# Performance work log

Measured on AMD Instinct MI355X. Metric: run time of the kernel, lower is better.

The kernel has to match this reference:

```python
import jax, jax.numpy as jnp
import numpy as np


def setup_inputs() -> dict:
    key = jax.random.key(0)
    k1, k2, k3, k4 = jax.random.split(key, 4)
    B, D, N, M = 4, 256, 4096, 4096
    return {
        "src": jax.random.normal(k1, (B, 3, N), dtype=jnp.float32),
        "tgt": jax.random.normal(k2, (B, 3, M), dtype=jnp.float32),
        "src_emb": jax.random.normal(k3, (B, D, N), dtype=jnp.float32),
        "tgt_emb": jax.random.normal(k4, (B, D, M), dtype=jnp.float32),
    }


def reference(src, tgt, src_emb, tgt_emb):
    # pairwise_distance[b,n,m] = -||src_emb[:,n] - tgt_emb[:,m]||^2
    # decomposed as -xx + 2*inner - yy (inner below is -2*dot, as in torch code)
    inner = -2.0 * jnp.einsum("bdn,bdm->bnm", src_emb, tgt_emb)       # [B,N,M]
    xx = jnp.sum(src_emb ** 2, axis=1)[:, :, None]                     # [B,N,1]
    yy = jnp.sum(tgt_emb ** 2, axis=1)[:, None, :]                     # [B,1,M]
    pairwise_distance = -xx - inner - yy                               # [B,N,M]
    scores = jax.nn.softmax(pairwise_distance, axis=2)                 # softmax over tgt points
    # src_corr[b,c,n] = sum_m tgt[b,c,m] * scores[b,n,m]
    src_corr = jnp.einsum("bcm,bnm->bcn", tgt, scores)                 # [B,3,N]
    return src_corr
```

## Files before the change

### kernel.cpp

```cpp
#include <hip/hip_runtime.h>

#define NBATCH 4
#define DDIM   256
#define NN     4096
#define MM     4096
#define NCHUNK 8
#define MCHUNK 512
#define MTILE  32
#define LOG2E  1.44269504088896340736f

using half8   = __attribute__((ext_vector_type(8))) _Float16;
using floatx4 = __attribute__((ext_vector_type(4))) float;


__global__ __launch_bounds__(256) void k_prep(const float* __restrict__ src_emb,
                                              const float* __restrict__ tgt_emb,
                                              const float* __restrict__ tgt,
                                              _Float16* __restrict__ Qf,
                                              _Float16* __restrict__ Kf,
                                              float* __restrict__ yyS,
                                              float4* __restrict__ Vt) {
    __shared__ float psum[4][256];
    int i = blockIdx.x;
    int tensor = i & 1, b = (i >> 1) & 3, dg = (i >> 3) & 1, ng = i >> 4;
    int t = threadIdx.x, w = t >> 6, lane = t & 63;
    int ds = dg * 4 + w;
    const float* in = tensor ? tgt_emb : src_emb;
    _Float16* outp  = tensor ? Kf : Qf;
    const float scale = tensor ? 1.0f : 2.0f * LOG2E;

    const float* ibase = in + ((size_t)b * DDIM + ds * 32) * NN + ng * 256;
    float4 f[4][8];
#pragma unroll
    for (int oct = 0; oct < 4; oct++)
#pragma unroll
        for (int k = 0; k < 8; k++)
            f[oct][k] = ((const float4*)(ibase + (size_t)(oct * 8 + k) * NN))[lane];

    half8* ob = (half8*)(outp + (size_t)b * NN * DDIM);
    int n0 = ng * 256 + lane * 4;
    float ss0 = 0.f, ss1 = 0.f, ss2 = 0.f, ss3 = 0.f;
#pragma unroll
    for (int oct = 0; oct < 4; oct++) {
        half8 v[4];
#pragma unroll
        for (int k = 0; k < 8; k++) {
            float4 g = f[oct][k];
            ss0 = fmaf(g.x, g.x, ss0);  ss1 = fmaf(g.y, g.y, ss1);
            ss2 = fmaf(g.z, g.z, ss2);  ss3 = fmaf(g.w, g.w, ss3);
            v[0][k] = (_Float16)(g.x * scale);
            v[1][k] = (_Float16)(g.y * scale);
            v[2][k] = (_Float16)(g.z * scale);
            v[3][k] = (_Float16)(g.w * scale);
        }
#pragma unroll
        for (int j = 0; j < 4; j++) {
            int n = n0 + j;
            ob[(((size_t)(n >> 4) * 8 + ds) * 4 + oct) * 16 + (n & 15)] = v[j];
        }
    }
    if (tensor) {
        psum[w][lane * 4 + 0] = ss0;  psum[w][lane * 4 + 1] = ss1;
        psum[w][lane * 4 + 2] = ss2;  psum[w][lane * 4 + 3] = ss3;
        __syncthreads();
        int m = ng * 256 + t;
        float s = (psum[0][t] + psum[1][t]) + (psum[2][t] + psum[3][t]);
        s *= -LOG2E;
        if (dg == 0) {
            const float* tp = tgt + (size_t)b * 3 * MM + m;
            Vt[(size_t)b * MM + m] = make_float4(tp[0], tp[MM], tp[2 * MM], s);
        } else {
            yyS[(size_t)b * MM + m] = s;
        }
    }
}

__global__ __launch_bounds__(256, 4) void k_flash(const _Float16* __restrict__ Qf,
                                                  const _Float16* __restrict__ Kf,
                                                  const float* __restrict__ yyS,
                                                  const float4* __restrict__ Vt,
                                                  float4* __restrict__ Opart,
                                                  float* __restrict__ Mpart) {
    __shared__ __align__(16) _Float16 Kt[2][MTILE * DDIM];
    __shared__ floatx4 vtt[MCHUNK];

    int i = blockIdx.x, t = threadIdx.x;
    int xcd = i & 7, j = i >> 3;
    int b = xcd >> 1, nhalf = xcd & 1;
    int chunk = j & 7, ntile = nhalf * 16 + (j >> 3);

    int wave = t >> 6, lane = t & 63, quad = lane >> 4, l15 = lane & 15;
    int m0 = chunk * MCHUNK;
    int mblk0 = m0 >> 4;

    const char* kfb = (const char*)(Kf + (size_t)b * NN * DDIM);
    auto stage = [&](int mt) {
        const char* gb = kfb + (size_t)(mblk0 + mt * 2) * 8192 + wave * 4096;
        char* lb = (char*)&Kt[mt & 1][0] + wave * 4096;
#pragma unroll
        for (int it = 0; it < 4; it++) {
            __builtin_amdgcn_global_load_lds(
                (const __attribute__((address_space(1))) uint32_t*)(const void*)
                    (gb + it * 1024 + lane * 16),
                (__attribute__((address_space(3))) uint32_t*)(void*)
                    (lb + it * 1024),
                16, 0, 0);
        }
    };

    stage(0);

    {
        const float4* vb = Vt + (size_t)b * MM + m0;
        const float* yb = yyS + (size_t)b * MM + m0;
        for (int r = t; r < MCHUNK; r += 256) {
            float4 g = vb[r];
            vtt[r] = (floatx4){g.x, g.y, g.z, g.w + yb[r]};
        }
    }

    int nblk0 = ntile * 8 + wave * 2;
    const half8* qp = (const half8*)Qf + (size_t)b * NN * 32;
    half8 qf[2][8];
#pragma unroll
    for (int nb = 0; nb < 2; nb++)
#pragma unroll
        for (int ds = 0; ds < 8; ds++)
            qf[nb][ds] = qp[(((size_t)(nblk0 + nb) * 8 + ds) * 4 + quad) * 16 + l15];

    const floatx4 z4 = {0.f, 0.f, 0.f, 0.f};
    floatx4 o[2] = {z4, z4};
    float mr[2] = {-__builtin_inff(), -__builtin_inff()};

    for (int mt = 0; mt < MCHUNK / MTILE; mt++) {
        __syncthreads();
        if (mt + 1 < MCHUNK / MTILE) stage(mt + 1);

        const char* Kb = (const char*)&Kt[mt & 1][0];
#pragma unroll
        for (int mb = 0; mb < 2; mb++) {
            const char* rb = Kb + mb * 8192 + lane * 16;
            floatx4 acc[2] = {z4, z4};
#pragma unroll
            for (int ds = 0; ds < 8; ds++) {
                half8 a = *(const half8*)(rb + ds * 1024);
                acc[0] = __builtin_amdgcn_mfma_f32_16x16x32_f16(a, qf[0][ds], acc[0], 0, 0, 0);
                acc[1] = __builtin_amdgcn_mfma_f32_16x16x32_f16(a, qf[1][ds], acc[1], 0, 0, 0);
            }

            floatx4 vr[4];
#pragma unroll
            for (int r = 0; r < 4; r++) vr[r] = vtt[mt * MTILE + mb * 16 + quad * 4 + r];
#pragma unroll
            for (int nb = 0; nb < 2; nb++) {
                float s[4];
#pragma unroll
                for (int r = 0; r < 4; r++) s[r] = acc[nb][r] + vr[r][3];
                float tm = fmaxf(fmaxf(s[0], s[1]), fmaxf(s[2], s[3]));
                float mn = fmaxf(mr[nb], tm);
                float al = __builtin_amdgcn_exp2f(mr[nb] - mn);
                mr[nb] = mn;
                o[nb] = o[nb] * al;
#pragma unroll
                for (int r = 0; r < 4; r++) {
                    float p = __builtin_amdgcn_exp2f(s[r] - mn);
                    o[nb][0] = fmaf(p, vr[r][0], o[nb][0]);
                    o[nb][1] = fmaf(p, vr[r][1], o[nb][1]);
                    o[nb][2] = fmaf(p, vr[r][2], o[nb][2]);
                    o[nb][3] += p;
                }
            }
        }
    }

#pragma unroll
    for (int nb = 0; nb < 2; nb++) {
        float mq = mr[nb];
        float ma = fmaxf(mq, __shfl_xor(mq, 16, 64));
        ma = fmaxf(ma, __shfl_xor(ma, 32, 64));
        float wgt = __builtin_amdgcn_exp2f(mq - ma);
        floatx4 ow = o[nb] * wgt;
#pragma unroll
        for (int c = 0; c < 4; c++) {
            float v = ow[c];
            v += __shfl_xor(v, 16, 64);
            v += __shfl_xor(v, 32, 64);
            ow[c] = v;
        }
        if (quad == 0) {
            int n = (nblk0 + nb) * 16 + l15;
            size_t idx = (size_t)(chunk * NBATCH + b) * NN + n;
            Opart[idx] = make_float4(ow[0], ow[1], ow[2], ow[3]);
            Mpart[idx] = ma;
        }
    }
}

__global__ __launch_bounds__(128) void k_combine(const float4* __restrict__ Opart,
                                                 const float* __restrict__ Mpart,
                                                 float* __restrict__ out) {
    int idx = blockIdx.x * 128 + threadIdx.x;
    int b = idx >> 12, n = idx & (NN - 1);
    float mstar = -__builtin_inff();
#pragma unroll
    for (int j = 0; j < NCHUNK; j++)
        mstar = fmaxf(mstar, Mpart[(size_t)(j * NBATCH + b) * NN + n]);
    float o0 = 0.f, o1 = 0.f, o2 = 0.f, l = 0.f;
#pragma unroll
    for (int j = 0; j < NCHUNK; j++) {
        size_t id = (size_t)(j * NBATCH + b) * NN + n;
        float w = __builtin_amdgcn_exp2f(Mpart[id] - mstar);
        float4 P = Opart[id];
        o0 = fmaf(w, P.x, o0); o1 = fmaf(w, P.y, o1);
        o2 = fmaf(w, P.z, o2); l  = fmaf(w, P.w, l);
    }
    out[(size_t)(b * 3 + 0) * NN + n] = o0 / l;
    out[(size_t)(b * 3 + 1) * NN + n] = o1 / l;
    out[(size_t)(b * 3 + 2) * NN + n] = o2 / l;
}

extern "C" void kernel_launch(void* const* d_in, const int* in_sizes, int n_in,
                              void* d_out, int out_size, void* d_ws, size_t ws_size,
                              hipStream_t stream) {
    const float* tgt     = (const float*)d_in[1];
    const float* src_emb = (const float*)d_in[2];
    const float* tgt_emb = (const float*)d_in[3];
    float* out = (float*)d_out;

    char* ws = (char*)d_ws;
    _Float16* Qf  = (_Float16*)(ws);
    _Float16* Kf  = (_Float16*)(ws + 8388608);
    float*    yyS = (float*)   (ws + 16777216);
    float4*   Vt  = (float4*)  (ws + 16842752);
    float4*   Op  = (float4*)  (ws + 17104896);
    float*    Mp  = (float*)   (ws + 19202048);

    hipLaunchKernelGGL(k_prep,    dim3(256),  dim3(256), 0, stream,
                       src_emb, tgt_emb, tgt, Qf, Kf, yyS, Vt);
    hipLaunchKernelGGL(k_flash,   dim3(1024), dim3(256), 0, stream, Qf, Kf, yyS, Vt, Op, Mp);
    hipLaunchKernelGGL(k_combine, dim3(128),  dim3(128), 0, stream, Op, Mp, out);
}
```

Measured before the change: 132.4 us.

## Stage prep loads via LDS DMA and batch online-softmax max per 32-column tile

The prep kernel now loads embeddings straight into LDS with global_load_lds over four times as many smaller blocks, then transposes and converts them from shared memory. This replaces the register-heavy float4 loads. In the flash kernel, the running-max rescale is done once per 32-wide M tile instead of once per 16-wide sub-tile, and both MFMA sub-tiles are issued before any softmax work. An empty asm constraint keeps the Q fragments in registers. This cuts exp and rescale work and increases MFMA overlap, at the cost of more live accumulator registers.

```diff
diff --git a/kernel.cpp b/kernel.cpp
--- a/kernel.cpp
+++ b/kernel.cpp
@@ -20,57 +20,59 @@
                                               _Float16* __restrict__ Kf,
                                               float* __restrict__ yyS,
                                               float4* __restrict__ Vt) {
-    __shared__ float psum[4][256];
+    __shared__ __align__(16) float tile[128 * 64];
+    __shared__ float psum[4][64];
     int i = blockIdx.x;
     int tensor = i & 1, b = (i >> 1) & 3, dg = (i >> 3) & 1, ng = i >> 4;
     int t = threadIdx.x, w = t >> 6, lane = t & 63;
-    int ds = dg * 4 + w;
     const float* in = tensor ? tgt_emb : src_emb;
     _Float16* outp  = tensor ? Kf : Qf;
     const float scale = tensor ? 1.0f : 2.0f * LOG2E;
 
-    const float* ibase = in + ((size_t)b * DDIM + ds * 32) * NN + ng * 256;
-    float4 f[4][8];
-#pragma unroll
-    for (int oct = 0; oct < 4; oct++)
-#pragma unroll
-        for (int k = 0; k < 8; k++)
-            f[oct][k] = ((const float4*)(ibase + (size_t)(oct * 8 + k) * NN))[lane];
-
+    const char* gb = (const char*)(in + ((size_t)b * DDIM + dg * 128 + w * 32) * NN + ng * 64);
+    char* lb = (char*)tile + w * 8192;
+#pragma unroll
+    for (int it = 0; it < 8; it++) {
+        __builtin_amdgcn_global_load_lds(
+            (const __attribute__((address_space(1))) uint32_t*)(const void*)
+                (gb + (size_t)(it * 4 + (lane >> 4)) * (NN * 4) + (lane & 15) * 16),
+            (__attribute__((address_space(3))) uint32_t*)(void*)
+                (lb + it * 1024),
+            16, 0, 0);
+    }
+    __syncthreads();
+
+    float ss = 0.f;
     half8* ob = (half8*)(outp + (size_t)b * NN * DDIM);
-    int n0 = ng * 256 + lane * 4;
-    float ss0 = 0.f, ss1 = 0.f, ss2 = 0.f, ss3 = 0.f;
-#pragma unroll
-    for (int oct = 0; oct < 4; oct++) {
-        half8 v[4];
+    int n_glob = ng * 64 + lane;
+    int blk = n_glob >> 4, l15 = n_glob & 15;
+#pragma unroll
+    for (int q = 0; q < 4; q++) {
+        int octg = w * 4 + q;
+        half8 v;
 #pragma unroll
         for (int k = 0; k < 8; k++) {
-            float4 g = f[oct][k];
-            ss0 = fmaf(g.x, g.x, ss0);  ss1 = fmaf(g.y, g.y, ss1);
-            ss2 = fmaf(g.z, g.z, ss2);  ss3 = fmaf(g.w, g.w, ss3);
-            v[0][k] = (_Float16)(g.x * scale);
-            v[1][k] = (_Float16)(g.y * scale);
-            v[2][k] = (_Float16)(g.z * scale);
-            v[3][k] = (_Float16)(g.w * scale);
-        }
-#pragma unroll
-        for (int j = 0; j < 4; j++) {
-            int n = n0 + j;
-            ob[(((size_t)(n >> 4) * 8 + ds) * 4 + oct) * 16 + (n & 15)] = v[j];
-        }
+            float f = tile[(octg * 8 + k) * 64 + lane];
+            ss = fmaf(f, f, ss);
+            v[k] = (_Float16)(f * scale);
+        }
+        int dglob = dg * 128 + octg * 8;
+        int dsg = dglob >> 5, oct = (dglob >> 3) & 3;
+        ob[(((size_t)blk * 8 + dsg) * 4 + oct) * 16 + l15] = v;
     }
     if (tensor) {
-        psum[w][lane * 4 + 0] = ss0;  psum[w][lane * 4 + 1] = ss1;
-        psum[w][lane * 4 + 2] = ss2;  psum[w][lane * 4 + 3] = ss3;
+        psum[w][lane] = ss;
         __syncthreads();
-        int m = ng * 256 + t;
-        float s = (psum[0][t] + psum[1][t]) + (psum[2][t] + psum[3][t]);
-        s *= -LOG2E;
-        if (dg == 0) {
-            const float* tp = tgt + (size_t)b * 3 * MM + m;
-            Vt[(size_t)b * MM + m] = make_float4(tp[0], tp[MM], tp[2 * MM], s);
-        } else {
-            yyS[(size_t)b * MM + m] = s;
+        if (t < 64) {
+            float s = psum[0][t] + psum[1][t] + psum[2][t] + psum[3][t];
+            s *= -LOG2E;
+            int m = ng * 64 + t;
+            if (dg == 0) {
+                const float* tp = tgt + (size_t)b * 3 * MM + m;
+                Vt[(size_t)b * MM + m] = make_float4(tp[0], tp[MM], tp[2 * MM], s);
+            } else {
+                yyS[(size_t)b * MM + m] = s;
+            }
         }
     }
 }
@@ -127,6 +129,11 @@
 #pragma unroll
         for (int ds = 0; ds < 8; ds++)
             qf[nb][ds] = qp[(((size_t)(nblk0 + nb) * 8 + ds) * 4 + quad) * 16 + l15];
+#pragma unroll
+    for (int nb = 0; nb < 2; nb++)
+#pragma unroll
+        for (int ds = 0; ds < 8; ds++)
+            asm volatile("" : "+v"(qf[nb][ds]));
 
     const floatx4 z4 = {0.f, 0.f, 0.f, 0.f};
     floatx4 o[2] = {z4, z4};
@@ -137,38 +144,51 @@
         if (mt + 1 < MCHUNK / MTILE) stage(mt + 1);
 
         const char* Kb = (const char*)&Kt[mt & 1][0];
+        floatx4 acc[2][2] = {{z4, z4}, {z4, z4}};
 #pragma unroll
         for (int mb = 0; mb < 2; mb++) {
             const char* rb = Kb + mb * 8192 + lane * 16;
-            floatx4 acc[2] = {z4, z4};
 #pragma unroll
             for (int ds = 0; ds < 8; ds++) {
                 half8 a = *(const half8*)(rb + ds * 1024);
-                acc[0] = __builtin_amdgcn_mfma_f32_16x16x32_f16(a, qf[0][ds], acc[0], 0, 0, 0);
-                acc[1] = __builtin_amdgcn_mfma_f32_16x16x32_f16(a, qf[1][ds], acc[1], 0, 0, 0);
-            }
-
-            floatx4 vr[4];
-#pragma unroll
-            for (int r = 0; r < 4; r++) vr[r] = vtt[mt * MTILE + mb * 16 + quad * 4 + r];
+                acc[mb][0] = __builtin_amdgcn_mfma_f32_16x16x32_f16(a, qf[0][ds], acc[mb][0], 0, 0, 0);
+                acc[mb][1] = __builtin_amdgcn_mfma_f32_16x16x32_f16(a, qf[1][ds], acc[mb][1], 0, 0, 0);
+            }
+        }
+
+        int vbase = mt * MTILE;
+        float yv[8];
+#pragma unroll
+        for (int r = 0; r < 4; r++) {
+            yv[r]     = ((const float*)&vtt[vbase + quad * 4 + r])[3];
+            yv[4 + r] = ((const float*)&vtt[vbase + 16 + quad * 4 + r])[3];
+        }
+#pragma unroll
+        for (int nb = 0; nb < 2; nb++) {
+#pragma unroll
+            for (int r = 0; r < 4; r++) {
+                acc[0][nb][r] += yv[r];
+                acc[1][nb][r] += yv[4 + r];
+            }
+            float tm = fmaxf(fmaxf(fmaxf(acc[0][nb][0], acc[0][nb][1]),
+                                   fmaxf(acc[0][nb][2], acc[0][nb][3])),
+                             fmaxf(fmaxf(acc[1][nb][0], acc[1][nb][1]),
+                                   fmaxf(acc[1][nb][2], acc[1][nb][3])));
+            float mn = fmaxf(mr[nb], tm);
+            float al = __builtin_amdgcn_exp2f(mr[nb] - mn);
+            mr[nb] = mn;
+            o[nb] = o[nb] * al;
+        }
+#pragma unroll
+        for (int jj = 0; jj < 8; jj++) {
+            floatx4 vr = vtt[vbase + (jj >> 2) * 16 + quad * 4 + (jj & 3)];
 #pragma unroll
             for (int nb = 0; nb < 2; nb++) {
-                float s[4];
-#pragma unroll
-                for (int r = 0; r < 4; r++) s[r] = acc[nb][r] + vr[r][3];
-                float tm = fmaxf(fmaxf(s[0], s[1]), fmaxf(s[2], s[3]));
-                float mn = fmaxf(mr[nb], tm);
-                float al = __builtin_amdgcn_exp2f(mr[nb] - mn);
-                mr[nb] = mn;
-                o[nb] = o[nb] * al;
-#pragma unroll
-                for (int r = 0; r < 4; r++) {
-                    float p = __builtin_amdgcn_exp2f(s[r] - mn);
-                    o[nb][0] = fmaf(p, vr[r][0], o[nb][0]);
-                    o[nb][1] = fmaf(p, vr[r][1], o[nb][1]);
-                    o[nb][2] = fmaf(p, vr[r][2], o[nb][2]);
-                    o[nb][3] += p;
-                }
+                float p = __builtin_amdgcn_exp2f(acc[jj >> 2][nb][jj & 3] - mr[nb]);
+                o[nb][0] = fmaf(p, vr[0], o[nb][0]);
+                o[nb][1] = fmaf(p, vr[1], o[nb][1]);
+                o[nb][2] = fmaf(p, vr[2], o[nb][2]);
+                o[nb][3] += p;
             }
         }
     }
@@ -235,7 +255,7 @@
     float4*   Op  = (float4*)  (ws + 17104896);
     float*    Mp  = (float*)   (ws + 19202048);
 
-    hipLaunchKernelGGL(k_prep,    dim3(256),  dim3(256), 0, stream,
+    hipLaunchKernelGGL(k_prep,    dim3(1024), dim3(256), 0, stream,
                        src_emb, tgt_emb, tgt, Qf, Kf, yyS, Vt);
     hipLaunchKernelGGL(k_flash,   dim3(1024), dim3(256), 0, stream, Qf, Kf, yyS, Vt, Op, Mp);
     hipLaunchKernelGGL(k_combine, dim3(128),  dim3(128), 0, stream, Op, Mp, out);
```

Result: no change. 133.9 us (+1.2%).
